# Optimization experiments

Measured on AMD Instinct MI355X. Metric: run time of the kernel, lower is better.

## Reference

```python
import jax, jax.numpy as jnp
import numpy as np

B, S, H, NH, HD, L, FF, E, V, K = 2, 1024, 1024, 16, 64, 4, 2560, 4, 32000, 2
EPS = 1e-5
ROPE_BASE = 10000.0


def setup_inputs() -> dict:
    key = jax.random.key(0)
    ks = jax.random.split(key, 16)
    s = 0.02
    inp = {}
    inp['input_ids'] = jax.random.randint(ks[0], (B, S), 0, V, dtype=jnp.int32)
    inp['token_emb'] = jax.random.normal(ks[1], (V, H), jnp.float32) * s
    inp['norm1_w'] = jnp.ones((L, H), jnp.float32)
    inp['wq'] = jax.random.normal(ks[2], (L, H, NH * HD), jnp.float32) * s
    inp['wk'] = jax.random.normal(ks[3], (L, H, NH * HD), jnp.float32) * s
    inp['wv'] = jax.random.normal(ks[4], (L, H, NH * HD), jnp.float32) * s
    inp['wo'] = jax.random.normal(ks[5], (L, NH * HD, H), jnp.float32) * s
    inp['norm2_w'] = jnp.ones((L, H), jnp.float32)
    inp['gate_w'] = jax.random.normal(ks[6], (L, H, E), jnp.float32) * s
    inp['gate_b'] = jnp.zeros((L, E), jnp.float32)
    inp['eg_w'] = jax.random.normal(ks[7], (L, E, H, FF), jnp.float32) * s
    inp['eg_b'] = jnp.zeros((L, E, FF), jnp.float32)
    inp['eu_w'] = jax.random.normal(ks[8], (L, E, H, FF), jnp.float32) * s
    inp['eu_b'] = jnp.zeros((L, E, FF), jnp.float32)
    inp['ed_w'] = jax.random.normal(ks[9], (L, E, FF, H), jnp.float32) * s
    inp['ed_b'] = jnp.zeros((L, E, H), jnp.float32)
    inp['normf_w'] = jnp.ones((H,), jnp.float32)
    inp['lm_head'] = jax.random.normal(ks[10], (H, V), jnp.float32) * s
    return inp


def _rmsnorm(x, w):
    return x * jax.lax.rsqrt(jnp.mean(x * x, axis=-1, keepdims=True) + EPS) * w


def _rope_tables():
    # precompute_freqs_cis: theta = base^{-(2i/HD)}, angles = outer(pos, theta)
    theta = 1.0 / (ROPE_BASE ** (jnp.arange(0, HD, 2, dtype=jnp.float32) / HD))  # [HD/2]
    pos = jnp.arange(S, dtype=jnp.float32)
    ang = jnp.outer(pos, theta)  # [S, HD/2]
    return jnp.cos(ang), jnp.sin(ang)


def _apply_rope(x, cos, sin):
    # x: [B, S, nh, HD]; torch view(b,s,h,2,HD/2) splits head_dim into two halves
    d = HD // 2
    x1, x2 = x[..., :d], x[..., d:]
    c = cos[None, :, None, :]
    s_ = sin[None, :, None, :]
    return jnp.concatenate([x1 * c - x2 * s_, x1 * s_ + x2 * c], axis=-1)


def reference(input_ids, token_emb, norm1_w, wq, wk, wv, wo, norm2_w,
              gate_w, gate_b, eg_w, eg_b, eu_w, eu_b, ed_w, ed_b,
              normf_w, lm_head):
    cos, sin = _rope_tables()
    neg = jnp.asarray(-1e9, jnp.float32)
    causal = jnp.where(jnp.tril(jnp.ones((S, S), bool)), 0.0, neg)  # [S,S]
    emb_scale = np.sqrt(float(H)).astype(np.float32)

    x = token_emb[input_ids] * emb_scale  # [B,S,H]
    bal = jnp.float32(0.0)
    inv_scale = np.float32(1.0 / np.sqrt(HD))

    for l in range(L):
        # --- attention block (pre-RMSNorm) ---
        h = _rmsnorm(x, norm1_w[l])
        q = (h @ wq[l]).reshape(B, S, NH, HD)
        k = (h @ wk[l]).reshape(B, S, NH, HD)
        v = (h @ wv[l]).reshape(B, S, NH, HD)
        q = _apply_rope(q, cos, sin)
        k = _apply_rope(k, cos, sin)
        scores = jnp.einsum('bqhd,bkhd->bhqk', q, k) * inv_scale + causal
        probs = jax.nn.softmax(scores, axis=-1)
        attn = jnp.einsum('bhqk,bkhd->bqhd', probs, v).reshape(B, S, NH * HD)
        x = x + attn @ wo[l]

        # --- MoE GEGLU feed-forward (pre-RMSNorm, top-2 routing) ---
        h2 = _rmsnorm(x, norm2_w[l]).reshape(-1, H)  # [T,H], T=B*S
        r_logits = h2 @ gate_w[l] + gate_b[l]
        r_probs = jax.nn.softmax(r_logits, axis=-1)
        vals, idx = jax.lax.top_k(r_probs, K)  # [T,K]
        vals = vals / jnp.sum(vals, axis=-1, keepdims=True)
        # dense combine weights [T,E]: renormalized top-k weight or 0
        comb = jnp.sum(jax.nn.one_hot(idx, E, dtype=h2.dtype) * vals[..., None], axis=1)
        gate = jax.nn.gelu(jnp.einsum('th,ehf->etf', h2, eg_w[l]) + eg_b[l][:, None, :],
                           approximate=False)
        up = jnp.einsum('th,ehf->etf', h2, eu_w[l]) + eu_b[l][:, None, :]
        eo = jnp.einsum('etf,efh->eth', gate * up, ed_w[l]) + ed_b[l][:, None, :]
        moe = jnp.einsum('eth,te->th', eo, comb).reshape(B, S, H)
        util = jnp.mean((comb > 0).astype(jnp.float32), axis=0)  # fraction of tokens per expert
        bal = bal + jnp.sum((util - 1.0 / E) ** 2)
        x = x + moe

    logits = _rmsnorm(x, normf_w) @ lm_head  # [B,S,V]
    return logits, bal
```

## Files before the change

### kernel.cpp

```cpp
#include <hip/hip_runtime.h>
#include <math.h>


typedef _Float16 f16;
typedef _Float16 f16x8 __attribute__((ext_vector_type(8)));
typedef _Float16 f16x4 __attribute__((ext_vector_type(4)));
typedef float f32x4 __attribute__((ext_vector_type(4)));

#define NT 2048
#define HH 1024
#define NHEAD 16
#define HDIM 64
#define NL 4
#define FFD 2560
#define NE 4
#define NV 32000
#define LMCH 6400

__device__ __forceinline__ void split_f32(float x, f16& h, f16& l) {
  h = (f16)x;
  l = (f16)((x - (float)h) * 2048.0f);
}

__global__ __launch_bounds__(256) void wsplit_kernel(
    const float* __restrict__ B, int ldb,
    f16* __restrict__ th, f16* __restrict__ tl, int K)
{
  __shared__ float t[32][33];
  const int bn = blockIdx.x * 32, bk = blockIdx.y * 32;
  const int c = threadIdx.x & 31, r0 = (threadIdx.x >> 5) * 4;
#pragma unroll
  for (int i = 0; i < 4; i++)
    t[r0 + i][c] = B[(size_t)(bk + r0 + i) * ldb + bn + c];
  __syncthreads();
#pragma unroll
  for (int i = 0; i < 4; i++) {
    int n = r0 + i;
    float v = t[c][n] * 256.0f;
    f16 h = (f16)v;
    f16 l = (f16)((v - (float)h) * 2048.0f);
    size_t o = (size_t)(bn + n) * K + bk + c;
    th[o] = h; tl[o] = l;
  }
}

#define BM 128
#define BN 128
#define BK 32
#define LDP 40

__global__ __launch_bounds__(256, 2) void gemm_split(
    const f16* __restrict__ Ahi, const f16* __restrict__ Alo,
    const f16* __restrict__ Bh, const f16* __restrict__ Bl,
    unsigned long long bstride,
    float* __restrict__ C0, float* __restrict__ C1, float* __restrict__ C2,
    const float* __restrict__ bias0, const float* __restrict__ bias1,
    const float* __restrict__ bias2,
    const float* __restrict__ rowscale, int rs_stride,
    int M, int N, int K, int ldc, int mode)
{
  const int z = blockIdx.z;
  const f16* Bhz = Bh + (size_t)z * bstride;
  const f16* Blz = Bl + (size_t)z * bstride;
  float* Cm = (z == 0) ? C0 : (z == 1 ? C1 : C2);
  const float* bz = (z == 0) ? bias0 : (z == 1 ? bias1 : bias2);

  __shared__ f16 AsH[BM * LDP], AsL[BM * LDP], BsH[BN * LDP], BsL[BN * LDP];

  const int tid = threadIdx.x;
  const int m0 = blockIdx.y * BM, n0 = blockIdx.x * BN;
  const int wave = tid >> 6, lane = tid & 63, quad = lane >> 4, l15 = lane & 15;
  const int wm = (wave >> 1) * 64, wn = (wave & 1) * 64;

  f32x4 acc0[4][4], acc1[4][4];
#pragma unroll
  for (int i = 0; i < 4; i++)
#pragma unroll
    for (int j = 0; j < 4; j++) {
      acc0[i][j] = (f32x4){0.f, 0.f, 0.f, 0.f};
      acc1[i][j] = (f32x4){0.f, 0.f, 0.f, 0.f};
    }

  for (int kt = 0; kt < K; kt += BK) {
#pragma unroll
    for (int i = 0; i < 2; i++) {
      int idx = tid + i * 256;
      int row = idx >> 2, col = (idx & 3) * 8;
      size_t ga = (size_t)(m0 + row) * K + kt + col;
      *(uint4*)&AsH[row * LDP + col] = *(const uint4*)&Ahi[ga];
      *(uint4*)&AsL[row * LDP + col] = *(const uint4*)&Alo[ga];
      size_t gb = (size_t)(n0 + row) * K + kt + col;
      *(uint4*)&BsH[row * LDP + col] = *(const uint4*)&Bhz[gb];
      *(uint4*)&BsL[row * LDP + col] = *(const uint4*)&Blz[gb];
    }
    __syncthreads();

    f16x8 bh[4], bl[4];
#pragma unroll
    for (int in = 0; in < 4; in++) {
      int r = wn + in * 16 + l15;
      bh[in] = *(const f16x8*)&BsH[r * LDP + quad * 8];
      bl[in] = *(const f16x8*)&BsL[r * LDP + quad * 8];
    }
#pragma unroll
    for (int im = 0; im < 4; im++) {
      int r = wm + im * 16 + l15;
      f16x8 ah = *(const f16x8*)&AsH[r * LDP + quad * 8];
      f16x8 al = *(const f16x8*)&AsL[r * LDP + quad * 8];
#pragma unroll
      for (int in = 0; in < 4; in++) {
        acc0[im][in] = __builtin_amdgcn_mfma_f32_16x16x32_f16(ah, bh[in], acc0[im][in], 0, 0, 0);
        acc1[im][in] = __builtin_amdgcn_mfma_f32_16x16x32_f16(ah, bl[in], acc1[im][in], 0, 0, 0);
        acc1[im][in] = __builtin_amdgcn_mfma_f32_16x16x32_f16(al, bh[in], acc1[im][in], 0, 0, 0);
      }
    }
    __syncthreads();
  }

  const float inv0 = 1.0f / 256.0f, inv1 = 1.0f / (256.0f * 2048.0f);
#pragma unroll
  for (int im = 0; im < 4; im++)
#pragma unroll
    for (int in = 0; in < 4; in++)
#pragma unroll
      for (int r = 0; r < 4; r++) {
        int row = m0 + wm + im * 16 + quad * 4 + r;
        int col = n0 + wn + in * 16 + l15;
        float v = acc0[im][in][r] * inv0 + acc1[im][in][r] * inv1;
        size_t o = (size_t)row * ldc + col;
        if (mode == 0) {
          if (bz) v += bz[col];
          Cm[o] = v;
        } else if (mode == 1) {
          Cm[o] += v;
        } else {
          v += bz[col];
          Cm[o] += rowscale[(size_t)row * rs_stride] * v;
        }
      }
}

__global__ __launch_bounds__(256, 2) void attn_kernel(
    const float* __restrict__ qf, const float* __restrict__ kf, const float* __restrict__ vf,
    f16* __restrict__ ohi, f16* __restrict__ olo)
{
  const int qblk = blockIdx.x, h = blockIdx.y, b = blockIdx.z;
  const int tid = threadIdx.x, wave = tid >> 6, lane = tid & 63;
  const int quad = lane >> 4, l15 = lane & 15;
  const int q0 = qblk * 64;
  const size_t bh_off = (size_t)b * 1024 * 1024 + (size_t)h * 64;

  __shared__ f16 KH[64 * 72], KL[64 * 72], VH[64 * 72], VL[64 * 72];
  __shared__ f16 PH[4][16 * 72], PL[4][16 * 72];

#pragma unroll
  for (int i = 0; i < 4; i++) {
    int idx = tid + i * 256;
    int row = idx >> 4, c4 = (idx & 15) * 4;
    float4 d = *(const float4*)&qf[bh_off + (size_t)(q0 + row) * 1024 + c4];
#pragma unroll
    for (int j = 0; j < 4; j++) {
      f16 hh, ll; split_f32(((const float*)&d)[j], hh, ll);
      KH[row * 72 + c4 + j] = hh;
      KL[row * 72 + c4 + j] = ll;
    }
  }
  __syncthreads();
  f16x8 qh[2], ql[2];
#pragma unroll
  for (int ks = 0; ks < 2; ks++) {
    qh[ks] = *(const f16x8*)&KH[(wave * 16 + l15) * 72 + ks * 32 + quad * 8];
    ql[ks] = *(const f16x8*)&KL[(wave * 16 + l15) * 72 + ks * 32 + quad * 8];
  }

  f32x4 o0[4], o1[4];
#pragma unroll
  for (int i = 0; i < 4; i++) { o0[i] = (f32x4){0.f,0.f,0.f,0.f}; o1[i] = (f32x4){0.f,0.f,0.f,0.f}; }
  float mrow[4] = {-3.0e38f, -3.0e38f, -3.0e38f, -3.0e38f};
  float lrow[4] = {0.f, 0.f, 0.f, 0.f};

  for (int kb = 0; kb <= qblk; kb++) {
    __syncthreads();
#pragma unroll
    for (int i = 0; i < 4; i++) {
      int idx = tid + i * 256;
      int row = idx >> 4, c4 = (idx & 15) * 4;
      float4 dk = *(const float4*)&kf[bh_off + (size_t)(kb * 64 + row) * 1024 + c4];
      float4 dv = *(const float4*)&vf[bh_off + (size_t)(kb * 64 + row) * 1024 + c4];
#pragma unroll
      for (int j = 0; j < 4; j++) {
        f16 hh, ll;
        split_f32(((const float*)&dk)[j], hh, ll);
        KH[row * 72 + c4 + j] = hh;  KL[row * 72 + c4 + j] = ll;
        split_f32(((const float*)&dv)[j], hh, ll);
        VH[(c4 + j) * 72 + row] = hh;  VL[(c4 + j) * 72 + row] = ll;
      }
    }
    __syncthreads();

    f32x4 s0[4], s1[4];
#pragma unroll
    for (int i = 0; i < 4; i++) { s0[i] = (f32x4){0.f,0.f,0.f,0.f}; s1[i] = (f32x4){0.f,0.f,0.f,0.f}; }
#pragma unroll
    for (int ks = 0; ks < 2; ks++) {
#pragma unroll
      for (int nt = 0; nt < 4; nt++) {
        f16x8 bhh = *(const f16x8*)&KH[(nt * 16 + l15) * 72 + ks * 32 + quad * 8];
        f16x8 bll = *(const f16x8*)&KL[(nt * 16 + l15) * 72 + ks * 32 + quad * 8];
        s0[nt] = __builtin_amdgcn_mfma_f32_16x16x32_f16(qh[ks], bhh, s0[nt], 0, 0, 0);
        s1[nt] = __builtin_amdgcn_mfma_f32_16x16x32_f16(qh[ks], bll, s1[nt], 0, 0, 0);
        s1[nt] = __builtin_amdgcn_mfma_f32_16x16x32_f16(ql[ks], bhh, s1[nt], 0, 0, 0);
      }
    }
    float sc[4][4], bm[4] = {-3.0e38f, -3.0e38f, -3.0e38f, -3.0e38f};
#pragma unroll
    for (int nt = 0; nt < 4; nt++)
#pragma unroll
      for (int r = 0; r < 4; r++) {
        float s = (s0[nt][r] + s1[nt][r] * (1.0f / 2048.0f)) * 0.125f;
        int kg = kb * 64 + nt * 16 + l15;
        int qg = q0 + wave * 16 + quad * 4 + r;
        if (kg > qg) s = -1.0e9f;
        sc[nt][r] = s;
        bm[r] = fmaxf(bm[r], s);
      }
#pragma unroll
    for (int r = 0; r < 4; r++) {
#pragma unroll
      for (int off = 1; off < 16; off <<= 1) bm[r] = fmaxf(bm[r], __shfl_xor(bm[r], off));
    }
    float alpha[4], ps[4] = {0.f, 0.f, 0.f, 0.f};
#pragma unroll
    for (int r = 0; r < 4; r++) {
      float mn = fmaxf(mrow[r], bm[r]);
      alpha[r] = expf(mrow[r] - mn);
      mrow[r] = mn;
    }
#pragma unroll
    for (int nt = 0; nt < 4; nt++)
#pragma unroll
      for (int r = 0; r < 4; r++) {
        float pv = expf(sc[nt][r] - mrow[r]);
        sc[nt][r] = pv;
        ps[r] += pv;
      }
#pragma unroll
    for (int r = 0; r < 4; r++) {
#pragma unroll
      for (int off = 1; off < 16; off <<= 1) ps[r] += __shfl_xor(ps[r], off);
      lrow[r] = lrow[r] * alpha[r] + ps[r];
    }
#pragma unroll
    for (int nt = 0; nt < 4; nt++)
#pragma unroll
      for (int r = 0; r < 4; r++) {
        f16 hh, ll; split_f32(sc[nt][r], hh, ll);
        PH[wave][(quad * 4 + r) * 72 + nt * 16 + l15] = hh;
        PL[wave][(quad * 4 + r) * 72 + nt * 16 + l15] = ll;
      }
#pragma unroll
    for (int dt = 0; dt < 4; dt++)
#pragma unroll
      for (int r = 0; r < 4; r++) { o0[dt][r] *= alpha[r]; o1[dt][r] *= alpha[r]; }
#pragma unroll
    for (int ks = 0; ks < 2; ks++) {
      f16x8 ah = *(const f16x8*)&PH[wave][l15 * 72 + ks * 32 + quad * 8];
      f16x8 al = *(const f16x8*)&PL[wave][l15 * 72 + ks * 32 + quad * 8];
#pragma unroll
      for (int dt = 0; dt < 4; dt++) {
        f16x8 bhh = *(const f16x8*)&VH[(dt * 16 + l15) * 72 + ks * 32 + quad * 8];
        f16x8 bll = *(const f16x8*)&VL[(dt * 16 + l15) * 72 + ks * 32 + quad * 8];
        o0[dt] = __builtin_amdgcn_mfma_f32_16x16x32_f16(ah, bhh, o0[dt], 0, 0, 0);
        o1[dt] = __builtin_amdgcn_mfma_f32_16x16x32_f16(ah, bll, o1[dt], 0, 0, 0);
        o1[dt] = __builtin_amdgcn_mfma_f32_16x16x32_f16(al, bhh, o1[dt], 0, 0, 0);
      }
    }
  }

#pragma unroll
  for (int dt = 0; dt < 4; dt++)
#pragma unroll
    for (int r = 0; r < 4; r++) {
      float o = (o0[dt][r] + o1[dt][r] * (1.0f / 2048.0f)) / lrow[r];
      int t = b * 1024 + q0 + wave * 16 + quad * 4 + r;
      size_t off = (size_t)t * 1024 + h * 64 + dt * 16 + l15;
      f16 hh, ll; split_f32(o, hh, ll);
      ohi[off] = hh; olo[off] = ll;
    }
}

__global__ __launch_bounds__(256) void rmsnorm_kernel(
    const float* __restrict__ x, const float* __restrict__ w,
    f16* __restrict__ ohi, f16* __restrict__ olo, float* __restrict__ of32)
{
  int t = blockIdx.x, tid = threadIdx.x;
  const float* xr = x + (size_t)t * HH;
  float4 xv = *(const float4*)&xr[tid * 4];
  float ss = xv.x * xv.x + xv.y * xv.y + xv.z * xv.z + xv.w * xv.w;
#pragma unroll
  for (int off = 32; off > 0; off >>= 1) ss += __shfl_down(ss, off);
  __shared__ float red[4];
  if ((tid & 63) == 0) red[tid >> 6] = ss;
  __syncthreads();
  float rs = 1.0f / sqrtf((red[0] + red[1] + red[2] + red[3]) * (1.0f / HH) + 1e-5f);
  float4 wv = *(const float4*)&w[tid * 4];
  float y0 = xv.x * rs * wv.x, y1 = xv.y * rs * wv.y;
  float y2 = xv.z * rs * wv.z, y3 = xv.w * rs * wv.w;
  f16 h0, l0, h1, l1, h2, l2, h3, l3;
  split_f32(y0, h0, l0); split_f32(y1, h1, l1);
  split_f32(y2, h2, l2); split_f32(y3, h3, l3);
  size_t o = (size_t)t * HH + tid * 4;
  *(f16x4*)&ohi[o] = (f16x4){h0, h1, h2, h3};
  *(f16x4*)&olo[o] = (f16x4){l0, l1, l2, l3};
  if (of32) *(float4*)&of32[o] = (float4){y0, y1, y2, y3};
}

__global__ __launch_bounds__(256) void embed_kernel(
    const int* __restrict__ ids, const float* __restrict__ emb, float* __restrict__ x)
{
  int t = blockIdx.x, tid = threadIdx.x;
  int v = ids[t];
  float4 d = *(const float4*)&emb[(size_t)v * HH + tid * 4];
  d.x *= 32.0f; d.y *= 32.0f; d.z *= 32.0f; d.w *= 32.0f;
  *(float4*)&x[(size_t)t * HH + tid * 4] = d;
}

__global__ __launch_bounds__(256) void rope_tables_kernel(float* __restrict__ cosT, float* __restrict__ sinT)
{
  int idx = blockIdx.x * 256 + threadIdx.x;
  int s = idx >> 5, j = idx & 31;
  double theta = pow(10000.0, -((double)(2 * j)) / 64.0);
  double ang = (double)s * theta;
  cosT[idx] = (float)cos(ang);
  sinT[idx] = (float)sin(ang);
}

__global__ __launch_bounds__(256) void rope_kernel(
    float* __restrict__ q, float* __restrict__ k,
    const float* __restrict__ cosT, const float* __restrict__ sinT)
{
  int idx = blockIdx.x * 256 + threadIdx.x;
  int j = idx & 31, h = (idx >> 5) & 15, t = idx >> 9;
  int s = t & 1023;
  float c = cosT[s * 32 + j], sn = sinT[s * 32 + j];
  size_t base = (size_t)t * HH + h * 64 + j;
  float q1 = q[base], q2 = q[base + 32];
  q[base] = q1 * c - q2 * sn;
  q[base + 32] = q1 * sn + q2 * c;
  float k1 = k[base], k2 = k[base + 32];
  k[base] = k1 * c - k2 * sn;
  k[base + 32] = k1 * sn + k2 * c;
}

__global__ __launch_bounds__(256) void gating_kernel(
    const float* __restrict__ h2f, const float* __restrict__ gw, const float* __restrict__ gb,
    float* __restrict__ comb, int* __restrict__ cnt)
{
  int t = blockIdx.x, tid = threadIdx.x;
  float4 xv = *(const float4*)&h2f[(size_t)t * HH + tid * 4];
  float4 w0 = *(const float4*)&gw[(size_t)(tid * 4 + 0) * 4];
  float4 w1 = *(const float4*)&gw[(size_t)(tid * 4 + 1) * 4];
  float4 w2 = *(const float4*)&gw[(size_t)(tid * 4 + 2) * 4];
  float4 w3 = *(const float4*)&gw[(size_t)(tid * 4 + 3) * 4];
  float a0 = xv.x * w0.x + xv.y * w1.x + xv.z * w2.x + xv.w * w3.x;
  float a1 = xv.x * w0.y + xv.y * w1.y + xv.z * w2.y + xv.w * w3.y;
  float a2 = xv.x * w0.z + xv.y * w1.z + xv.z * w2.z + xv.w * w3.z;
  float a3 = xv.x * w0.w + xv.y * w1.w + xv.z * w2.w + xv.w * w3.w;
#pragma unroll
  for (int off = 32; off > 0; off >>= 1) {
    a0 += __shfl_down(a0, off); a1 += __shfl_down(a1, off);
    a2 += __shfl_down(a2, off); a3 += __shfl_down(a3, off);
  }
  __shared__ float red[4][4];
  if ((tid & 63) == 0) { int w = tid >> 6; red[w][0] = a0; red[w][1] = a1; red[w][2] = a2; red[w][3] = a3; }
  __syncthreads();
  if (tid == 0) {
    float lg[4];
#pragma unroll
    for (int e = 0; e < 4; e++)
      lg[e] = red[0][e] + red[1][e] + red[2][e] + red[3][e] + gb[e];
    int e1 = 0;
    for (int e = 1; e < 4; e++) if (lg[e] > lg[e1]) e1 = e;
    int e2 = -1;
    for (int e = 0; e < 4; e++) if (e != e1 && (e2 < 0 || lg[e] > lg[e2])) e2 = e;
    float p2 = expf(lg[e2] - lg[e1]);
    float v1 = 1.0f / (1.0f + p2), v2 = p2 / (1.0f + p2);
    float c[4] = {0.f, 0.f, 0.f, 0.f};
    c[e1] = v1; c[e2] = v2;
    *(float4*)&comb[(size_t)t * 4] = (float4){c[0], c[1], c[2], c[3]};
    atomicAdd(&cnt[e1], 1);
    atomicAdd(&cnt[e2], 1);
  }
}

__global__ __launch_bounds__(256) void gelumul_kernel(
    const float* __restrict__ g, const float* __restrict__ u,
    f16* __restrict__ oh, f16* __restrict__ ol)
{
  size_t i = ((size_t)blockIdx.x * 256 + threadIdx.x) * 4;
  float4 gv = *(const float4*)&g[i];
  float4 uv = *(const float4*)&u[i];
  f16 h[4], l[4];
#pragma unroll
  for (int j = 0; j < 4; j++) {
    float xx = ((const float*)&gv)[j];
    float ge = 0.5f * xx * (1.0f + erff(xx * 0.70710678118654752f));
    float y = ge * ((const float*)&uv)[j];
    split_f32(y, h[j], l[j]);
  }
  *(f16x4*)&oh[i] = (f16x4){h[0], h[1], h[2], h[3]};
  *(f16x4*)&ol[i] = (f16x4){l[0], l[1], l[2], l[3]};
}

__global__ void zero_cnt_kernel(int* cnt) {
  if (threadIdx.x < 16) cnt[threadIdx.x] = 0;
}

__global__ void bal_kernel(const int* __restrict__ cnt, float* __restrict__ out) {
  if (threadIdx.x == 0) {
    float bal = 0.f;
    for (int l = 0; l < NL; l++)
      for (int e = 0; e < NE; e++) {
        float u = (float)cnt[l * NE + e] * (1.0f / (float)NT);
        float d = u - 0.25f;
        bal += d * d;
      }
    out[0] = bal;
  }
}

extern "C" void kernel_launch(void* const* d_in, const int* in_sizes, int n_in,
                              void* d_out, int out_size, void* d_ws, size_t ws_size,
                              hipStream_t stream)
{
  (void)in_sizes; (void)n_in; (void)out_size; (void)ws_size;
  const int*   ids  = (const int*)  d_in[0];
  const float* temb = (const float*)d_in[1];
  const float* n1w  = (const float*)d_in[2];
  const float* wq   = (const float*)d_in[3];
  const float* wk   = (const float*)d_in[4];
  const float* wv   = (const float*)d_in[5];
  const float* wo   = (const float*)d_in[6];
  const float* n2w  = (const float*)d_in[7];
  const float* gw   = (const float*)d_in[8];
  const float* gb   = (const float*)d_in[9];
  const float* egw  = (const float*)d_in[10];
  const float* egb  = (const float*)d_in[11];
  const float* euw  = (const float*)d_in[12];
  const float* eub  = (const float*)d_in[13];
  const float* edw  = (const float*)d_in[14];
  const float* edb  = (const float*)d_in[15];
  const float* nfw  = (const float*)d_in[16];
  const float* lmh  = (const float*)d_in[17];
  float* out = (float*)d_out;

  char* p = (char*)d_ws;
  auto carve = [&](size_t n) { char* r = p; p += (n + 255) & ~(size_t)255; return r; };
  float* x    = (float*)carve((size_t)NT * HH * 4);
  float* h2f  = (float*)carve((size_t)NT * HH * 4);
  f16*   hhi  = (f16*)  carve((size_t)NT * HH * 2);
  f16*   hlo  = (f16*)  carve((size_t)NT * HH * 2);
  f16*   ahi  = (f16*)  carve((size_t)NT * HH * 2);
  f16*   alo  = (f16*)  carve((size_t)NT * HH * 2);
  f16*   guh  = (f16*)  carve((size_t)NT * FFD * 2);
  f16*   gul  = (f16*)  carve((size_t)NT * FFD * 2);
  float* gbuf = (float*)carve((size_t)NT * FFD * 4);
  float* ubuf = (float*)carve((size_t)NT * FFD * 4);
  float* comb = (float*)carve((size_t)NT * NE * 4);
  int*   cnt  = (int*)  carve(64);
  float* cosT = (float*)carve((size_t)1024 * 32 * 4);
  float* sinT = (float*)carve((size_t)1024 * 32 * 4);
  const size_t WB = (size_t)LMCH * HH;
  f16* whi = (f16*)carve(WB * 2);
  f16* wlo = (f16*)carve(WB * 2);
  float* qf = gbuf;
  float* kf = gbuf + (size_t)NT * HH;
  float* vf = ubuf;

  zero_cnt_kernel<<<1, 64, 0, stream>>>(cnt);
  rope_tables_kernel<<<128, 256, 0, stream>>>(cosT, sinT);
  embed_kernel<<<NT, 256, 0, stream>>>(ids, temb, x);

  for (int l = 0; l < NL; l++) {
    rmsnorm_kernel<<<NT, 256, 0, stream>>>(x, n1w + (size_t)l * HH, hhi, hlo, nullptr);
    wsplit_kernel<<<dim3(HH/32, HH/32), 256, 0, stream>>>(wq + (size_t)l * HH * HH, HH, whi, wlo, HH);
    wsplit_kernel<<<dim3(HH/32, HH/32), 256, 0, stream>>>(wk + (size_t)l * HH * HH, HH, whi + (size_t)HH*HH, wlo + (size_t)HH*HH, HH);
    wsplit_kernel<<<dim3(HH/32, HH/32), 256, 0, stream>>>(wv + (size_t)l * HH * HH, HH, whi + (size_t)2*HH*HH, wlo + (size_t)2*HH*HH, HH);
    gemm_split<<<dim3(8, 16, 3), 256, 0, stream>>>(hhi, hlo,
        whi, wlo, (unsigned long long)HH * HH,
        qf, kf, vf, nullptr, nullptr, nullptr, nullptr, 0, NT, HH, HH, HH, 0);
    rope_kernel<<<4096, 256, 0, stream>>>(qf, kf, cosT, sinT);
    attn_kernel<<<dim3(16, 16, 2), 256, 0, stream>>>(qf, kf, vf, ahi, alo);
    wsplit_kernel<<<dim3(HH/32, HH/32), 256, 0, stream>>>(wo + (size_t)l * HH * HH, HH, whi, wlo, HH);
    gemm_split<<<dim3(8, 16, 1), 256, 0, stream>>>(ahi, alo,
        whi, wlo, 0,
        x, nullptr, nullptr, nullptr, nullptr, nullptr, nullptr, 0, NT, HH, HH, HH, 1);
    rmsnorm_kernel<<<NT, 256, 0, stream>>>(x, n2w + (size_t)l * HH, hhi, hlo, h2f);
    gating_kernel<<<NT, 256, 0, stream>>>(h2f, gw + (size_t)l * HH * NE, gb + (size_t)l * NE,
                                          comb, cnt + l * NE);
    for (int e = 0; e < NE; e++) {
      size_t wof = ((size_t)(l * NE + e)) * HH * FFD;
      size_t bof = (size_t)(l * NE + e) * FFD;
      wsplit_kernel<<<dim3(FFD/32, HH/32), 256, 0, stream>>>(egw + wof, FFD, whi, wlo, HH);
      wsplit_kernel<<<dim3(FFD/32, HH/32), 256, 0, stream>>>(euw + wof, FFD, whi + (size_t)HH*FFD, wlo + (size_t)HH*FFD, HH);
      gemm_split<<<dim3(20, 16, 2), 256, 0, stream>>>(hhi, hlo,
          whi, wlo, (unsigned long long)HH * FFD,
          gbuf, ubuf, nullptr,
          egb + bof, eub + bof, nullptr, nullptr, 0, NT, FFD, HH, FFD, 0);
      gelumul_kernel<<<(NT * FFD / 1024), 256, 0, stream>>>(gbuf, ubuf, guh, gul);
      wsplit_kernel<<<dim3(HH/32, FFD/32), 256, 0, stream>>>(edw + wof, HH, whi, wlo, FFD);
      gemm_split<<<dim3(8, 16, 1), 256, 0, stream>>>(guh, gul,
          whi, wlo, 0,
          x, nullptr, nullptr,
          edb + (size_t)(l * NE + e) * HH, nullptr, nullptr, comb + e, NE, NT, HH, FFD, HH, 2);
    }
  }
  rmsnorm_kernel<<<NT, 256, 0, stream>>>(x, nfw, hhi, hlo, nullptr);
  for (int ch = 0; ch < 5; ch++) {
    wsplit_kernel<<<dim3(LMCH/32, HH/32), 256, 0, stream>>>(lmh + (size_t)ch * LMCH, NV, whi, wlo, HH);
    gemm_split<<<dim3(LMCH/128, 16, 1), 256, 0, stream>>>(hhi, hlo,
        whi, wlo, 0,
        out + (size_t)ch * LMCH, nullptr, nullptr,
        nullptr, nullptr, nullptr, nullptr, 0, NT, LMCH, HH, NV, 0);
  }
  bal_kernel<<<1, 64, 0, stream>>>(cnt, out + (size_t)NT * NV);
}
```

Baseline: 6.410 ms.

## Route MoE expert GEMMs over only the tokens assigned to each expert

The gating kernel now builds per-expert token lists and counts with atomics. The expert up/gate GEMM gathers A rows through that list, the GELU-mul stops at the count, and the down GEMM scatters results back to the original token rows. Blocks beyond the count exit early. With top-2 of 4 experts this removes about half of the dense expert FLOPs, at the cost of an extra zeroing launch, indirect row addressing, and a nondeterministic token order within each list.

```diff
diff --git a/kernel.cpp b/kernel.cpp
--- a/kernel.cpp
+++ b/kernel.cpp
@@ -57,8 +57,15 @@
     const float* __restrict__ bias0, const float* __restrict__ bias1,
     const float* __restrict__ bias2,
     const float* __restrict__ rowscale, int rs_stride,
+    const int* __restrict__ gidxA, const int* __restrict__ gidxC,
+    const int* __restrict__ cntp,
     int M, int N, int K, int ldc, int mode)
 {
+  const int m0 = blockIdx.y * BM, n0 = blockIdx.x * BN;
+  int cnt = M;
+  if (cntp) cnt = *cntp;
+  if (m0 >= cnt) return;
+
   const int z = blockIdx.z;
   const f16* Bhz = Bh + (size_t)z * bstride;
   const f16* Blz = Bl + (size_t)z * bstride;
@@ -68,9 +75,21 @@
   __shared__ f16 AsH[BM * LDP], AsL[BM * LDP], BsH[BN * LDP], BsL[BN * LDP];
 
   const int tid = threadIdx.x;
-  const int m0 = blockIdx.y * BM, n0 = blockIdx.x * BN;
   const int wave = tid >> 6, lane = tid & 63, quad = lane >> 4, l15 = lane & 15;
   const int wm = (wave >> 1) * 64, wn = (wave & 1) * 64;
+
+  size_t arow[2], brow[2];
+  int scol[2];
+#pragma unroll
+  for (int i = 0; i < 2; i++) {
+    int idx = tid + i * 256;
+    int row = idx >> 2;
+    scol[i] = (idx & 3) * 8;
+    int gr = m0 + row;
+    if (gidxA) gr = gidxA[gr < cnt ? gr : cnt - 1];
+    arow[i] = (size_t)gr * K;
+    brow[i] = (size_t)(n0 + row) * K;
+  }
 
   f32x4 acc0[4][4], acc1[4][4];
 #pragma unroll
@@ -85,11 +104,11 @@
 #pragma unroll
     for (int i = 0; i < 2; i++) {
       int idx = tid + i * 256;
-      int row = idx >> 2, col = (idx & 3) * 8;
-      size_t ga = (size_t)(m0 + row) * K + kt + col;
+      int row = idx >> 2, col = scol[i];
+      size_t ga = arow[i] + kt + col;
       *(uint4*)&AsH[row * LDP + col] = *(const uint4*)&Ahi[ga];
       *(uint4*)&AsL[row * LDP + col] = *(const uint4*)&Alo[ga];
-      size_t gb = (size_t)(n0 + row) * K + kt + col;
+      size_t gb = brow[i] + kt + col;
       *(uint4*)&BsH[row * LDP + col] = *(const uint4*)&Bhz[gb];
       *(uint4*)&BsL[row * LDP + col] = *(const uint4*)&Blz[gb];
     }
@@ -124,10 +143,12 @@
     for (int in = 0; in < 4; in++)
 #pragma unroll
       for (int r = 0; r < 4; r++) {
-        int row = m0 + wm + im * 16 + quad * 4 + r;
+        int grow = m0 + wm + im * 16 + quad * 4 + r;
+        if (grow >= cnt) continue;
+        int orow = gidxC ? gidxC[grow] : grow;
         int col = n0 + wn + in * 16 + l15;
         float v = acc0[im][in][r] * inv0 + acc1[im][in][r] * inv1;
-        size_t o = (size_t)row * ldc + col;
+        size_t o = (size_t)orow * ldc + col;
         if (mode == 0) {
           if (bz) v += bz[col];
           Cm[o] = v;
@@ -135,7 +156,7 @@
           Cm[o] += v;
         } else {
           v += bz[col];
-          Cm[o] += rowscale[(size_t)row * rs_stride] * v;
+          Cm[o] += rowscale[(size_t)orow * rs_stride] * v;
         }
       }
 }
@@ -354,7 +375,8 @@
 
 __global__ __launch_bounds__(256) void gating_kernel(
     const float* __restrict__ h2f, const float* __restrict__ gw, const float* __restrict__ gb,
-    float* __restrict__ comb, int* __restrict__ cnt)
+    float* __restrict__ comb, int* __restrict__ cnt,
+    int* __restrict__ elist, int* __restrict__ ecnt)
 {
   int t = blockIdx.x, tid = threadIdx.x;
   float4 xv = *(const float4*)&h2f[(size_t)t * HH + tid * 4];
@@ -390,14 +412,19 @@
     *(float4*)&comb[(size_t)t * 4] = (float4){c[0], c[1], c[2], c[3]};
     atomicAdd(&cnt[e1], 1);
     atomicAdd(&cnt[e2], 1);
+    int p1 = atomicAdd(&ecnt[e1], 1);
+    elist[e1 * NT + p1] = t;
+    int pq = atomicAdd(&ecnt[e2], 1);
+    elist[e2 * NT + pq] = t;
   }
 }
 
 __global__ __launch_bounds__(256) void gelumul_kernel(
     const float* __restrict__ g, const float* __restrict__ u,
-    f16* __restrict__ oh, f16* __restrict__ ol)
+    f16* __restrict__ oh, f16* __restrict__ ol, const int* __restrict__ cntp)
 {
   size_t i = ((size_t)blockIdx.x * 256 + threadIdx.x) * 4;
+  if (cntp && i >= (size_t)(*cntp) * FFD) return;
   float4 gv = *(const float4*)&g[i];
   float4 uv = *(const float4*)&u[i];
   f16 h[4], l[4];
@@ -468,6 +495,8 @@
   float* ubuf = (float*)carve((size_t)NT * FFD * 4);
   float* comb = (float*)carve((size_t)NT * NE * 4);
   int*   cnt  = (int*)  carve(64);
+  int*   elist= (int*)  carve((size_t)NE * NT * 4);
+  int*   ecnt = (int*)  carve(64);
   float* cosT = (float*)carve((size_t)1024 * 32 * 4);
   float* sinT = (float*)carve((size_t)1024 * 32 * 4);
   const size_t WB = (size_t)LMCH * HH;
@@ -488,16 +517,19 @@
     wsplit_kernel<<<dim3(HH/32, HH/32), 256, 0, stream>>>(wv + (size_t)l * HH * HH, HH, whi + (size_t)2*HH*HH, wlo + (size_t)2*HH*HH, HH);
     gemm_split<<<dim3(8, 16, 3), 256, 0, stream>>>(hhi, hlo,
         whi, wlo, (unsigned long long)HH * HH,
-        qf, kf, vf, nullptr, nullptr, nullptr, nullptr, 0, NT, HH, HH, HH, 0);
+        qf, kf, vf, nullptr, nullptr, nullptr, nullptr, 0,
+        nullptr, nullptr, nullptr, NT, HH, HH, HH, 0);
     rope_kernel<<<4096, 256, 0, stream>>>(qf, kf, cosT, sinT);
     attn_kernel<<<dim3(16, 16, 2), 256, 0, stream>>>(qf, kf, vf, ahi, alo);
     wsplit_kernel<<<dim3(HH/32, HH/32), 256, 0, stream>>>(wo + (size_t)l * HH * HH, HH, whi, wlo, HH);
     gemm_split<<<dim3(8, 16, 1), 256, 0, stream>>>(ahi, alo,
         whi, wlo, 0,
-        x, nullptr, nullptr, nullptr, nullptr, nullptr, nullptr, 0, NT, HH, HH, HH, 1);
+        x, nullptr, nullptr, nullptr, nullptr, nullptr, nullptr, 0,
+        nullptr, nullptr, nullptr, NT, HH, HH, HH, 1);
     rmsnorm_kernel<<<NT, 256, 0, stream>>>(x, n2w + (size_t)l * HH, hhi, hlo, h2f);
+    zero_cnt_kernel<<<1, 64, 0, stream>>>(ecnt);
     gating_kernel<<<NT, 256, 0, stream>>>(h2f, gw + (size_t)l * HH * NE, gb + (size_t)l * NE,
-                                          comb, cnt + l * NE);
+                                          comb, cnt + l * NE, elist, ecnt);
     for (int e = 0; e < NE; e++) {
       size_t wof = ((size_t)(l * NE + e)) * HH * FFD;
       size_t bof = (size_t)(l * NE + e) * FFD;
@@ -506,13 +538,15 @@
       gemm_split<<<dim3(20, 16, 2), 256, 0, stream>>>(hhi, hlo,
           whi, wlo, (unsigned long long)HH * FFD,
           gbuf, ubuf, nullptr,
-          egb + bof, eub + bof, nullptr, nullptr, 0, NT, FFD, HH, FFD, 0);
-      gelumul_kernel<<<(NT * FFD / 1024), 256, 0, stream>>>(gbuf, ubuf, guh, gul);
+          egb + bof, eub + bof, nullptr, nullptr, 0,
+          elist + e * NT, nullptr, ecnt + e, NT, FFD, HH, FFD, 0);
+      gelumul_kernel<<<(NT * FFD / 1024), 256, 0, stream>>>(gbuf, ubuf, guh, gul, ecnt + e);
       wsplit_kernel<<<dim3(HH/32, FFD/32), 256, 0, stream>>>(edw + wof, HH, whi, wlo, FFD);
       gemm_split<<<dim3(8, 16, 1), 256, 0, stream>>>(guh, gul,
           whi, wlo, 0,
           x, nullptr, nullptr,
-          edb + (size_t)(l * NE + e) * HH, nullptr, nullptr, comb + e, NE, NT, HH, FFD, HH, 2);
+          edb + (size_t)(l * NE + e) * HH, nullptr, nullptr, comb + e, NE,
+          nullptr, elist + e * NT, ecnt + e, NT, HH, FFD, HH, 2);
     }
   }
   rmsnorm_kernel<<<NT, 256, 0, stream>>>(x, nfw, hhi, hlo, nullptr);
@@ -521,7 +555,8 @@
     gemm_split<<<dim3(LMCH/128, 16, 1), 256, 0, stream>>>(hhi, hlo,
         whi, wlo, 0,
         out + (size_t)ch * LMCH, nullptr, nullptr,
-        nullptr, nullptr, nullptr, nullptr, 0, NT, LMCH, HH, NV, 0);
+        nullptr, nullptr, nullptr, nullptr, 0,
+        nullptr, nullptr, nullptr, NT, LMCH, HH, NV, 0);
   }
   bal_kernel<<<1, 64, 0, stream>>>(cnt, out + (size_t)NT * NV);
 }
```

Result: faster. 6.019 ms (-6.1%).
